# Performance work log

Hardware: AMD Instinct MI355X
Metric: run time of the kernel (lower is better)

Reference implementation:

```python
import jax, jax.numpy as jnp
import numpy as np

N_NODES = 100000
N_EDGES = 1600000
N_GRAPHS = 256
NEG_SLOPE_GAT = 0.2   # GATConv default
NEG_SLOPE_ACT = 0.01  # F.leaky_relu default


def _leaky(x, s):
    return jnp.where(x >= 0, x, s * x)


def _gat_layer(x, src, dst, W, a_src, a_dst, b, n):
    # h = W x ; per-node attention logits
    h = x @ W                      # [N, D]
    al_s = h @ a_src               # [N]
    al_d = h @ a_dst               # [N]
    e = _leaky(al_s[src] + al_d[dst], NEG_SLOPE_GAT)  # [E]
    # segment softmax over incoming edges of each dst node
    m = jax.ops.segment_max(e, dst, num_segments=n)
    m = jnp.where(jnp.isfinite(m), m, 0.0)
    ex = jnp.exp(e - m[dst])
    s = jax.ops.segment_sum(ex, dst, num_segments=n)
    alpha = ex / (s[dst] + 1e-16)
    out = jax.ops.segment_sum(h[src] * alpha[:, None], dst, num_segments=n)
    return out + b


def setup_inputs() -> dict:
    key = jax.random.key(0)
    ks = jax.random.split(key, 12)
    x = jax.random.normal(ks[0], (N_NODES, 72), dtype=jnp.float32)
    edge_index = jax.random.randint(ks[1], (2, N_EDGES), 0, N_NODES, dtype=jnp.int64)
    batch = jnp.sort(jax.random.randint(ks[2], (N_NODES,), 0, N_GRAPHS, dtype=jnp.int64))
    def glorot(k, shape):
        fan = shape[0] + shape[-1]
        return jax.random.normal(k, shape, dtype=jnp.float32) * jnp.sqrt(2.0 / fan)
    return {
        "x": x, "edge_index": edge_index, "batch": batch,
        "W1": glorot(ks[3], (72, 64)),
        "a_src1": glorot(ks[4], (64,)), "a_dst1": glorot(ks[5], (64,)),
        "b1": jnp.zeros((64,), jnp.float32),
        "W2": glorot(ks[6], (64, 64)),
        "a_src2": glorot(ks[7], (64,)), "a_dst2": glorot(ks[8], (64,)),
        "b2": jnp.zeros((64,), jnp.float32),
        "fcW": glorot(ks[9], (64, 2)),
        "fcb": jnp.zeros((2,), jnp.float32),
    }


def reference(x, edge_index, batch, W1, a_src1, a_dst1, b1, W2, a_src2, a_dst2, b2, fcW, fcb):
    n = x.shape[0]
    # PyG GATConv adds self-loops by default
    loops = jnp.arange(n, dtype=edge_index.dtype)
    src = jnp.concatenate([edge_index[0], loops])
    dst = jnp.concatenate([edge_index[1], loops])
    h = _gat_layer(x, src, dst, W1, a_src1, a_dst1, b1, n)
    h = _leaky(h, NEG_SLOPE_ACT)
    h = _gat_layer(h, src, dst, W2, a_src2, a_dst2, b2, n)
    # global mean pool over graphs
    sums = jax.ops.segment_sum(h, batch, num_segments=N_GRAPHS)
    cnt = jax.ops.segment_sum(jnp.ones((n,), h.dtype), batch, num_segments=N_GRAPHS)
    pooled = sums / jnp.maximum(cnt, 1.0)[:, None]
    # dropout is identity at inference
    return pooled @ fcW + fcb
```

## Files before the change

kernel.cpp:

```cpp
#include <hip/hip_runtime.h>
#include <hip/hip_bf16.h>
#include <math.h>


#define NPB 256
#define EPB 4096

__device__ __forceinline__ void atomAddF(float* a, float v) {
    unsafeAtomicAdd(a, v);
}

__device__ __forceinline__ unsigned int f2bf(float v) {
    unsigned int b = __float_as_uint(v);
    b += 0x7FFFu + ((b >> 16) & 1u);
    return b >> 16;
}

__global__ __launch_bounds__(256) void init_all(float* __restrict__ pooled,
                                                float* __restrict__ cnt,
                                                int* __restrict__ bucket_cnt,
                                                int NB, int G) {
    int i = blockIdx.x * 256 + threadIdx.x;
    if (i < G * 64) pooled[i] = 0.0f;
    if (i < G) cnt[i] = 0.0f;
    if (i < NB) bucket_cnt[i] = 0;
}

__global__ __launch_bounds__(256) void bucket_hist(const int* __restrict__ ei,
                                                   int E, int NB,
                                                   int* __restrict__ bucket_cnt) {
    __shared__ int h[512];
    int t = threadIdx.x;
    for (int i = t; i < 512; i += 256) h[i] = 0;
    __syncthreads();
    int i0 = blockIdx.x * EPB;
#pragma unroll
    for (int k = 0; k < 16; k++) {
        int i = i0 + k * 256 + t;
        if (i < E) atomicAdd(&h[ei[E + i] >> 8], 1);
    }
    __syncthreads();
    for (int b = t; b < NB; b += 256)
        if (h[b]) atomicAdd(&bucket_cnt[b], h[b]);
}

__global__ __launch_bounds__(512) void scan_buckets(const int* __restrict__ cnt,
                                                    int* __restrict__ base,
                                                    int* __restrict__ cur, int NB) {
    __shared__ int tmp[512];
    int t = threadIdx.x;
    int v = (t < NB) ? cnt[t] : 0;
    tmp[t] = v;
    __syncthreads();
    for (int o = 1; o < 512; o <<= 1) {
        int u = (t >= o) ? tmp[t - o] : 0;
        __syncthreads();
        tmp[t] += u;
        __syncthreads();
    }
    if (t < NB) { int e = tmp[t] - v; base[t] = e; cur[t] = e; }
}

__global__ __launch_bounds__(256) void partition(const int* __restrict__ ei,
                                                 int E, int NB,
                                                 int* __restrict__ cur,
                                                 uint2* __restrict__ pairs) {
    __shared__ int h[512];
    __shared__ int bb[512];
    int t = threadIdx.x;
    for (int i = t; i < 512; i += 256) h[i] = 0;
    __syncthreads();
    int i0 = blockIdx.x * EPB;
    int s[16], bk[16], r[16];
#pragma unroll
    for (int k = 0; k < 16; k++) {
        int i = i0 + k * 256 + t;
        bk[k] = -1;
        if (i < E) {
            s[k] = ei[i];
            int d = ei[E + i];
            bk[k] = d >> 8;
            r[k] = atomicAdd(&h[bk[k]], 1);
        }
    }
    __syncthreads();
    for (int b = t; b < NB; b += 256)
        bb[b] = h[b] ? atomicAdd(&cur[b], h[b]) : 0;
    __syncthreads();
#pragma unroll
    for (int k = 0; k < 16; k++) {
        if (bk[k] < 0) continue;
        int i = i0 + k * 256 + t;
        int d = ei[E + i];
        pairs[bb[bk[k]] + r[k]] = make_uint2((unsigned)s[k], (unsigned)d);
    }
}

__global__ __launch_bounds__(256) void build_csr(const uint2* __restrict__ pairs,
                                                 const int* __restrict__ cnt,
                                                 const int* __restrict__ base,
                                                 int n, int tot,
                                                 int* __restrict__ rowptr,
                                                 int* __restrict__ srcs) {
    int b = blockIdx.x, t = threadIdx.x;
    int d0 = b << 8;
    int nb = min(NPB, n - d0);
    int pbeg = base[b], pend = pbeg + cnt[b];
    int csr0 = pbeg + d0;

    __shared__ int deg[NPB];
    __shared__ int cur[NPB];
    __shared__ int tmp[NPB];
    deg[t] = (t < nb) ? 1 : 0;
    __syncthreads();
    for (int j = pbeg + t; j < pend; j += 256)
        atomicAdd(&deg[pairs[j].y - d0], 1);
    __syncthreads();
    int v = deg[t];
    tmp[t] = v;
    __syncthreads();
    for (int o = 1; o < NPB; o <<= 1) {
        int u = (t >= o) ? tmp[t - o] : 0;
        __syncthreads();
        tmp[t] += u;
        __syncthreads();
    }
    int excl = tmp[t] - v;
    if (t < nb) {
        rowptr[d0 + t] = csr0 + excl;
        srcs[csr0 + excl] = d0 + t;
        cur[t] = excl + 1;
    }
    __syncthreads();
    for (int j = pbeg + t; j < pend; j += 256) {
        uint2 p = pairs[j];
        int off = atomicAdd(&cur[p.y - d0], 1);
        srcs[csr0 + off] = (int)p.x;
    }
    if (b == 0 && t == 0) rowptr[n] = tot;
}

template <int IN_DIM>
__global__ __launch_bounds__(256) void node_gemm(const float* __restrict__ x,
                                                 const float* __restrict__ W,
                                                 const float* __restrict__ a_src,
                                                 const float* __restrict__ a_dst,
                                                 const float* __restrict__ bias_in,
                                                 float slope_in,
                                                 unsigned short* __restrict__ h16,
                                                 float* __restrict__ al_s,
                                                 float* __restrict__ al_d,
                                                 int n) {
    __shared__ float Ws[IN_DIM * 64];
    __shared__ float xs[IN_DIM][64];
    int t = threadIdx.x;
    int nbase = blockIdx.x * 64;

    for (int idx = t; idx < IN_DIM * 16; idx += 256)
        ((float4*)Ws)[idx] = ((const float4*)W)[idx];
    for (int idx = t; idx < IN_DIM * 64; idx += 256) {
        int node = nbase + (idx & 63);
        int k = idx >> 6;
        float v = 0.0f;
        if (node < n) {
            v = x[(size_t)node * IN_DIM + k];
            if (bias_in) {
                v += bias_in[k];
                v = (v >= 0.0f) ? v : slope_in * v;
            }
        }
        xs[k][idx & 63] = v;
    }
    __syncthreads();

    int cg = t & 15;
    int ng = t >> 4;
    float acc[4][4] = {};
#pragma unroll 8
    for (int k = 0; k < IN_DIM; k++) {
        float4 xv = *(const float4*)&xs[k][ng * 4];
        float4 wv = *(const float4*)&Ws[k * 64 + cg * 4];
        float xa[4] = {xv.x, xv.y, xv.z, xv.w};
        float wa[4] = {wv.x, wv.y, wv.z, wv.w};
#pragma unroll
        for (int i = 0; i < 4; i++)
#pragma unroll
            for (int j = 0; j < 4; j++)
                acc[i][j] += xa[i] * wa[j];
    }

    float4 as4 = *(const float4*)(a_src + cg * 4);
    float4 ad4 = *(const float4*)(a_dst + cg * 4);
#pragma unroll
    for (int i = 0; i < 4; i++) {
        int node = nbase + ng * 4 + i;
        if (node < n) {
            uint2 p;
            p.x = f2bf(acc[i][0]) | (f2bf(acc[i][1]) << 16);
            p.y = f2bf(acc[i][2]) | (f2bf(acc[i][3]) << 16);
            *(uint2*)(h16 + (size_t)node * 64 + cg * 4) = p;
        }
        float vs = acc[i][0] * as4.x + acc[i][1] * as4.y +
                   acc[i][2] * as4.z + acc[i][3] * as4.w;
        float vd = acc[i][0] * ad4.x + acc[i][1] * ad4.y +
                   acc[i][2] * ad4.z + acc[i][3] * ad4.w;
#pragma unroll
        for (int o = 8; o; o >>= 1) {
            vs += __shfl_xor(vs, o);
            vd += __shfl_xor(vd, o);
        }
        if (cg == 0 && node < n) { al_s[node] = vs; al_d[node] = vd; }
    }
}

__device__ __forceinline__ void bf8_fma(float* acc, uint4 q, float w) {
    acc[0] += w * __uint_as_float(q.x << 16);
    acc[1] += w * __uint_as_float(q.x & 0xFFFF0000u);
    acc[2] += w * __uint_as_float(q.y << 16);
    acc[3] += w * __uint_as_float(q.y & 0xFFFF0000u);
    acc[4] += w * __uint_as_float(q.z << 16);
    acc[5] += w * __uint_as_float(q.z & 0xFFFF0000u);
    acc[6] += w * __uint_as_float(q.w << 16);
    acc[7] += w * __uint_as_float(q.w & 0xFFFF0000u);
}

__global__ __launch_bounds__(256) void gat_aggregate(const int* __restrict__ rowptr,
                                                     const int* __restrict__ srcs,
                                                     const float* __restrict__ als,
                                                     const float* __restrict__ ald,
                                                     const unsigned short* __restrict__ h16,
                                                     float* __restrict__ hout,
                                                     int n) {
    int t = threadIdx.x;
    int sub = t >> 3, lane = t & 7;
    int node = blockIdx.x * 32 + sub;
    if (node >= n) return;
    int beg = rowptr[node], end = rowptr[node + 1];
    float aldv = ald[node];

    float acc[8] = {};
    float sm = 0.0f;
    int j = beg;
    for (; j + 4 <= end; j += 4) {
        int s0 = srcs[j], s1 = srcs[j + 1], s2 = srcs[j + 2], s3 = srcs[j + 3];
        float e0 = als[s0] + aldv, e1 = als[s1] + aldv;
        float e2 = als[s2] + aldv, e3 = als[s3] + aldv;
        uint4 q0 = *(const uint4*)(h16 + (size_t)s0 * 64 + lane * 8);
        uint4 q1 = *(const uint4*)(h16 + (size_t)s1 * 64 + lane * 8);
        uint4 q2 = *(const uint4*)(h16 + (size_t)s2 * 64 + lane * 8);
        uint4 q3 = *(const uint4*)(h16 + (size_t)s3 * 64 + lane * 8);
        e0 = (e0 >= 0.0f) ? e0 : 0.2f * e0;
        e1 = (e1 >= 0.0f) ? e1 : 0.2f * e1;
        e2 = (e2 >= 0.0f) ? e2 : 0.2f * e2;
        e3 = (e3 >= 0.0f) ? e3 : 0.2f * e3;
        float w0 = __expf(e0), w1 = __expf(e1);
        float w2 = __expf(e2), w3 = __expf(e3);
        sm += (w0 + w1) + (w2 + w3);
        bf8_fma(acc, q0, w0);
        bf8_fma(acc, q1, w1);
        bf8_fma(acc, q2, w2);
        bf8_fma(acc, q3, w3);
    }
    for (; j < end; j++) {
        int s = srcs[j];
        float e = als[s] + aldv;
        e = (e >= 0.0f) ? e : 0.2f * e;
        float w = __expf(e);
        uint4 q = *(const uint4*)(h16 + (size_t)s * 64 + lane * 8);
        sm += w;
        bf8_fma(acc, q, w);
    }

    float inv = 1.0f / (sm + 1e-16f);
    float4 o0 = make_float4(acc[0] * inv, acc[1] * inv, acc[2] * inv, acc[3] * inv);
    float4 o1 = make_float4(acc[4] * inv, acc[5] * inv, acc[6] * inv, acc[7] * inv);
    float* op = hout + (size_t)node * 64 + lane * 8;
    *(float4*)op = o0;
    *(float4*)(op + 4) = o1;
}

__global__ __launch_bounds__(256) void pool_run(const float* __restrict__ hout,
                                                const float* __restrict__ b2,
                                                const int* __restrict__ batch,
                                                float* __restrict__ pooled,
                                                float* __restrict__ cnt,
                                                int n) {
    int t = threadIdx.x;
    int wv = blockIdx.x * 4 + (t >> 6);
    int lane = t & 63;
    int start = wv * 64;
    if (start >= n) return;
    int end = min(start + 64, n);
    float bb = b2[lane];
    int gcur = batch[start];
    float acc = 0.0f;
    int rl = 0;
    for (int node = start; node < end; node++) {
        int g = batch[node];
        if (g != gcur) {
            atomAddF(&pooled[gcur * 64 + lane], acc);
            if (lane == 0) atomAddF(&cnt[gcur], (float)rl);
            acc = 0.0f; rl = 0; gcur = g;
        }
        acc += hout[(size_t)node * 64 + lane] + bb;
        rl++;
    }
    atomAddF(&pooled[gcur * 64 + lane], acc);
    if (lane == 0) atomAddF(&cnt[gcur], (float)rl);
}

__global__ __launch_bounds__(64) void final_fc(const float* __restrict__ pooled,
                                               const float* __restrict__ cnt,
                                               const float* __restrict__ fcW,
                                               const float* __restrict__ fcb,
                                               float* __restrict__ out) {
    int g = blockIdx.x;
    int lane = threadIdx.x;
    float c = cnt[g];
    c = (c > 1.0f) ? c : 1.0f;
    float p = pooled[g * 64 + lane] / c;
    float s0 = p * fcW[lane * 2 + 0];
    float s1 = p * fcW[lane * 2 + 1];
#pragma unroll
    for (int o = 32; o; o >>= 1) {
        s0 += __shfl_xor(s0, o);
        s1 += __shfl_xor(s1, o);
    }
    if (lane == 0) {
        out[g * 2 + 0] = s0 + fcb[0];
        out[g * 2 + 1] = s1 + fcb[1];
    }
}

extern "C" void kernel_launch(void* const* d_in, const int* in_sizes, int n_in,
                              void* d_out, int out_size, void* d_ws, size_t ws_size,
                              hipStream_t stream) {
    const float* x    = (const float*)d_in[0];
    const int*   ei   = (const int*)d_in[1];
    const int*   batch= (const int*)d_in[2];
    const float* W1   = (const float*)d_in[3];
    const float* as1  = (const float*)d_in[4];
    const float* ad1  = (const float*)d_in[5];
    const float* b1   = (const float*)d_in[6];
    const float* W2   = (const float*)d_in[7];
    const float* as2  = (const float*)d_in[8];
    const float* ad2  = (const float*)d_in[9];
    const float* b2   = (const float*)d_in[10];
    const float* fcW  = (const float*)d_in[11];
    const float* fcb  = (const float*)d_in[12];
    float* out = (float*)d_out;

    const int N = in_sizes[2];
    const int E = in_sizes[1] / 2;
    const int G = out_size / 2;
    const int tot = E + N;
    const int NB = (N + NPB - 1) / NPB;

    float* ws     = (float*)d_ws;
    float* bufO   = ws;
    uint2* pairs  = (uint2*)(bufO + (size_t)N * 64);
    float* als    = (float*)(pairs + E);
    float* ald    = als + N;
    float* pooled = ald + N;
    float* cnt    = pooled + (size_t)G * 64;
    int*   rowptr = (int*)(cnt + G);
    int*   srcs   = rowptr + N + 1;
    int*   bcnt   = srcs + tot;
    int*   bbase  = bcnt + NB;
    int*   bcur   = bbase + NB;
    unsigned short* bufH16 = (unsigned short*)(bcur + NB);

    dim3 b256(256);
    int gInit = (max(G * 64, NB) + 255) / 256;
    int gPart = (E + EPB - 1) / EPB;
    int gGemm = (N + 63) / 64;
    int gAgg  = (N + 31) / 32;
    int gPool = ((N + 63) / 64 + 3) / 4;

    init_all<<<gInit, b256, 0, stream>>>(pooled, cnt, bcnt, NB, G);
    bucket_hist<<<gPart, b256, 0, stream>>>(ei, E, NB, bcnt);
    scan_buckets<<<1, 512, 0, stream>>>(bcnt, bbase, bcur, NB);
    partition<<<gPart, b256, 0, stream>>>(ei, E, NB, bcur, pairs);
    build_csr<<<NB, b256, 0, stream>>>(pairs, bcnt, bbase, N, tot, rowptr, srcs);

    node_gemm<72><<<gGemm, b256, 0, stream>>>(x, W1, as1, ad1, nullptr, 0.0f,
                                              bufH16, als, ald, N);
    gat_aggregate<<<gAgg, b256, 0, stream>>>(rowptr, srcs, als, ald, bufH16, bufO, N);

    node_gemm<64><<<gGemm, b256, 0, stream>>>(bufO, W2, as2, ad2, b1, 0.01f,
                                              bufH16, als, ald, N);
    gat_aggregate<<<gAgg, b256, 0, stream>>>(rowptr, srcs, als, ald, bufH16, bufO, N);

    pool_run<<<gPool, b256, 0, stream>>>(bufO, b2, batch, pooled, cnt, N);
    final_fc<<<G, 64, 0, stream>>>(pooled, cnt, fcW, fcb, out);
}
```

Measured before the change: 348.9 us.

## Precompute edge weights and sort nodes by degree for balanced aggregation

Adds a separate edge_weights pass that computes exp(leaky(als[src]+ald[dst])) per edge and stores it packed with the source index. The aggregation kernel then reads these packed pairs instead of recomputing logits. It also builds a degree-bucketed permutation of nodes (histogram, scan, scatter), so each block's 8-lane groups handle nodes of similar degree, reducing load imbalance within wavefronts. The cost is extra kernel launches and an additional pass over the edges that writes and rereads 8 bytes per edge. The permutation also scatters output writes.

```diff
diff --git a/kernel.cpp b/kernel.cpp
--- a/kernel.cpp
+++ b/kernel.cpp
@@ -19,11 +19,13 @@
 __global__ __launch_bounds__(256) void init_all(float* __restrict__ pooled,
                                                 float* __restrict__ cnt,
                                                 int* __restrict__ bucket_cnt,
+                                                int* __restrict__ bins,
                                                 int NB, int G) {
     int i = blockIdx.x * 256 + threadIdx.x;
     if (i < G * 64) pooled[i] = 0.0f;
     if (i < G) cnt[i] = 0.0f;
     if (i < NB) bucket_cnt[i] = 0;
+    if (i < 64) bins[i] = 0;
 }
 
 __global__ __launch_bounds__(256) void bucket_hist(const int* __restrict__ ei,
@@ -138,6 +140,57 @@
         srcs[csr0 + off] = (int)p.x;
     }
     if (b == 0 && t == 0) rowptr[n] = tot;
+}
+
+__global__ __launch_bounds__(256) void perm_hist(const int* __restrict__ rowptr,
+                                                 int n, int* __restrict__ bins) {
+    __shared__ int h[64];
+    int t = threadIdx.x;
+    if (t < 64) h[t] = 0;
+    __syncthreads();
+    int i = blockIdx.x * 256 + t;
+    if (i < n) {
+        int d = min(rowptr[i + 1] - rowptr[i], 64) - 1;
+        atomicAdd(&h[d], 1);
+    }
+    __syncthreads();
+    if (t < 64 && h[t]) atomicAdd(&bins[t], h[t]);
+}
+
+__global__ __launch_bounds__(64) void perm_scan(const int* __restrict__ bins,
+                                                int* __restrict__ cur) {
+    __shared__ int tmp[64];
+    int t = threadIdx.x;
+    int v = bins[t];
+    tmp[t] = v;
+    __syncthreads();
+    for (int o = 1; o < 64; o <<= 1) {
+        int u = (t >= o) ? tmp[t - o] : 0;
+        __syncthreads();
+        tmp[t] += u;
+        __syncthreads();
+    }
+    cur[t] = tmp[t] - v;
+}
+
+__global__ __launch_bounds__(256) void perm_scatter(const int* __restrict__ rowptr,
+                                                    int n, int* __restrict__ cur,
+                                                    int* __restrict__ perm) {
+    __shared__ int h[64];
+    __shared__ int bb[64];
+    int t = threadIdx.x;
+    if (t < 64) h[t] = 0;
+    __syncthreads();
+    int i = blockIdx.x * 256 + t;
+    int b = -1, r = 0;
+    if (i < n) {
+        b = min(rowptr[i + 1] - rowptr[i], 64) - 1;
+        r = atomicAdd(&h[b], 1);
+    }
+    __syncthreads();
+    if (t < 64) bb[t] = h[t] ? atomicAdd(&cur[t], h[t]) : 0;
+    __syncthreads();
+    if (i < n) perm[bb[b] + r] = i;
 }
 
 template <int IN_DIM>
@@ -213,6 +266,25 @@
     }
 }
 
+__global__ __launch_bounds__(256) void edge_weights(const int* __restrict__ rowptr,
+                                                    const int* __restrict__ srcs,
+                                                    const float* __restrict__ als,
+                                                    const float* __restrict__ ald,
+                                                    uint2* __restrict__ ew, int n) {
+    int t = threadIdx.x;
+    int sub = t >> 3, lane = t & 7;
+    int node = blockIdx.x * 32 + sub;
+    if (node >= n) return;
+    float adv = ald[node];
+    int beg = rowptr[node], end = rowptr[node + 1];
+    for (int j = beg + lane; j < end; j += 8) {
+        int s = srcs[j];
+        float e = als[s] + adv;
+        e = (e >= 0.0f) ? e : 0.2f * e;
+        ew[j] = make_uint2((unsigned)s, __float_as_uint(__expf(e)));
+    }
+}
+
 __device__ __forceinline__ void bf8_fma(float* acc, uint4 q, float w) {
     acc[0] += w * __uint_as_float(q.x << 16);
     acc[1] += w * __uint_as_float(q.x & 0xFFFF0000u);
@@ -225,36 +297,29 @@
 }
 
 __global__ __launch_bounds__(256) void gat_aggregate(const int* __restrict__ rowptr,
-                                                     const int* __restrict__ srcs,
-                                                     const float* __restrict__ als,
-                                                     const float* __restrict__ ald,
+                                                     const int* __restrict__ perm,
+                                                     const uint2* __restrict__ ew,
                                                      const unsigned short* __restrict__ h16,
                                                      float* __restrict__ hout,
                                                      int n) {
     int t = threadIdx.x;
     int sub = t >> 3, lane = t & 7;
-    int node = blockIdx.x * 32 + sub;
-    if (node >= n) return;
+    int r = blockIdx.x * 32 + sub;
+    if (r >= n) return;
+    int node = perm[r];
     int beg = rowptr[node], end = rowptr[node + 1];
-    float aldv = ald[node];
 
     float acc[8] = {};
     float sm = 0.0f;
     int j = beg;
     for (; j + 4 <= end; j += 4) {
-        int s0 = srcs[j], s1 = srcs[j + 1], s2 = srcs[j + 2], s3 = srcs[j + 3];
-        float e0 = als[s0] + aldv, e1 = als[s1] + aldv;
-        float e2 = als[s2] + aldv, e3 = als[s3] + aldv;
-        uint4 q0 = *(const uint4*)(h16 + (size_t)s0 * 64 + lane * 8);
-        uint4 q1 = *(const uint4*)(h16 + (size_t)s1 * 64 + lane * 8);
-        uint4 q2 = *(const uint4*)(h16 + (size_t)s2 * 64 + lane * 8);
-        uint4 q3 = *(const uint4*)(h16 + (size_t)s3 * 64 + lane * 8);
-        e0 = (e0 >= 0.0f) ? e0 : 0.2f * e0;
-        e1 = (e1 >= 0.0f) ? e1 : 0.2f * e1;
-        e2 = (e2 >= 0.0f) ? e2 : 0.2f * e2;
-        e3 = (e3 >= 0.0f) ? e3 : 0.2f * e3;
-        float w0 = __expf(e0), w1 = __expf(e1);
-        float w2 = __expf(e2), w3 = __expf(e3);
+        uint2 e0 = ew[j], e1 = ew[j + 1], e2 = ew[j + 2], e3 = ew[j + 3];
+        uint4 q0 = *(const uint4*)(h16 + (size_t)e0.x * 64 + lane * 8);
+        uint4 q1 = *(const uint4*)(h16 + (size_t)e1.x * 64 + lane * 8);
+        uint4 q2 = *(const uint4*)(h16 + (size_t)e2.x * 64 + lane * 8);
+        uint4 q3 = *(const uint4*)(h16 + (size_t)e3.x * 64 + lane * 8);
+        float w0 = __uint_as_float(e0.y), w1 = __uint_as_float(e1.y);
+        float w2 = __uint_as_float(e2.y), w3 = __uint_as_float(e3.y);
         sm += (w0 + w1) + (w2 + w3);
         bf8_fma(acc, q0, w0);
         bf8_fma(acc, q1, w1);
@@ -262,11 +327,9 @@
         bf8_fma(acc, q3, w3);
     }
     for (; j < end; j++) {
-        int s = srcs[j];
-        float e = als[s] + aldv;
-        e = (e >= 0.0f) ? e : 0.2f * e;
-        float w = __expf(e);
-        uint4 q = *(const uint4*)(h16 + (size_t)s * 64 + lane * 8);
+        uint2 e = ew[j];
+        float w = __uint_as_float(e.y);
+        uint4 q = *(const uint4*)(h16 + (size_t)e.x * 64 + lane * 8);
         sm += w;
         bf8_fma(acc, q, w);
     }
@@ -359,7 +422,8 @@
     float* ws     = (float*)d_ws;
     float* bufO   = ws;
     uint2* pairs  = (uint2*)(bufO + (size_t)N * 64);
-    float* als    = (float*)(pairs + E);
+    uint2* ew     = pairs;
+    float* als    = (float*)(pairs + tot);
     float* ald    = als + N;
     float* pooled = ald + N;
     float* cnt    = pooled + (size_t)G * 64;
@@ -368,28 +432,37 @@
     int*   bcnt   = srcs + tot;
     int*   bbase  = bcnt + NB;
     int*   bcur   = bbase + NB;
-    unsigned short* bufH16 = (unsigned short*)(bcur + NB);
+    int*   bins   = bcur + NB;
+    int*   pcur   = bins + 64;
+    int*   perm   = pcur + 64;
+    unsigned short* bufH16 = (unsigned short*)(perm + N);
 
     dim3 b256(256);
     int gInit = (max(G * 64, NB) + 255) / 256;
     int gPart = (E + EPB - 1) / EPB;
+    int gNB   = (N + 255) / 256;
     int gGemm = (N + 63) / 64;
     int gAgg  = (N + 31) / 32;
     int gPool = ((N + 63) / 64 + 3) / 4;
 
-    init_all<<<gInit, b256, 0, stream>>>(pooled, cnt, bcnt, NB, G);
+    init_all<<<gInit, b256, 0, stream>>>(pooled, cnt, bcnt, bins, NB, G);
     bucket_hist<<<gPart, b256, 0, stream>>>(ei, E, NB, bcnt);
     scan_buckets<<<1, 512, 0, stream>>>(bcnt, bbase, bcur, NB);
     partition<<<gPart, b256, 0, stream>>>(ei, E, NB, bcur, pairs);
     build_csr<<<NB, b256, 0, stream>>>(pairs, bcnt, bbase, N, tot, rowptr, srcs);
+    perm_hist<<<gNB, b256, 0, stream>>>(rowptr, N, bins);
+    perm_scan<<<1, 64, 0, stream>>>(bins, pcur);
+    perm_scatter<<<gNB, b256, 0, stream>>>(rowptr, N, pcur, perm);
 
     node_gemm<72><<<gGemm, b256, 0, stream>>>(x, W1, as1, ad1, nullptr, 0.0f,
                                               bufH16, als, ald, N);
-    gat_aggregate<<<gAgg, b256, 0, stream>>>(rowptr, srcs, als, ald, bufH16, bufO, N);
+    edge_weights<<<gAgg, b256, 0, stream>>>(rowptr, srcs, als, ald, ew, N);
+    gat_aggregate<<<gAgg, b256, 0, stream>>>(rowptr, perm, ew, bufH16, bufO, N);
 
     node_gemm<64><<<gGemm, b256, 0, stream>>>(bufO, W2, as2, ad2, b1, 0.01f,
                                               bufH16, als, ald, N);
-    gat_aggregate<<<gAgg, b256, 0, stream>>>(rowptr, srcs, als, ald, bufH16, bufO, N);
+    edge_weights<<<gAgg, b256, 0, stream>>>(rowptr, srcs, als, ald, ew, N);
+    gat_aggregate<<<gAgg, b256, 0, stream>>>(rowptr, perm, ew, bufH16, bufO, N);
 
     pool_run<<<gPool, b256, 0, stream>>>(bufO, b2, batch, pooled, cnt, N);
     final_fc<<<G, 64, 0, stream>>>(pooled, cnt, fcW, fcb, out);
```

After: 400.7 us. 14.9% more time.

## Split GAT aggregation into two feature-half passes with 4 lanes per node

Applied to the files above, without the earlier changes.

The aggregation kernel now handles half of the 64 features per launch, with 4 threads per node instead of 8, and runs twice per layer (phase 0 and 1). The aim is to shrink the gathered working set per pass (32 bf16 features per source row) so it fits better in cache during the random gathers. The cost is that the edge list, attention logits and exp are read and computed twice, and there are extra kernel launches.

```diff
diff --git a/kernel.cpp b/kernel.cpp
--- a/kernel.cpp
+++ b/kernel.cpp
@@ -224,19 +224,21 @@
     acc[7] += w * __uint_as_float(q.w & 0xFFFF0000u);
 }
 
-__global__ __launch_bounds__(256) void gat_aggregate(const int* __restrict__ rowptr,
-                                                     const int* __restrict__ srcs,
-                                                     const float* __restrict__ als,
-                                                     const float* __restrict__ ald,
-                                                     const unsigned short* __restrict__ h16,
-                                                     float* __restrict__ hout,
-                                                     int n) {
-    int t = threadIdx.x;
-    int sub = t >> 3, lane = t & 7;
-    int node = blockIdx.x * 32 + sub;
+__global__ __launch_bounds__(256) void gat_aggregate_half(
+        const int* __restrict__ rowptr,
+        const int* __restrict__ srcs,
+        const float* __restrict__ als,
+        const float* __restrict__ ald,
+        const unsigned short* __restrict__ h16,
+        float* __restrict__ hout,
+        int n, int phase) {
+    int t = threadIdx.x;
+    int sub = t >> 2, lane = t & 3;
+    int node = blockIdx.x * 64 + sub;
     if (node >= n) return;
     int beg = rowptr[node], end = rowptr[node + 1];
     float aldv = ald[node];
+    const unsigned short* hb = h16 + phase * 32 + lane * 8;
 
     float acc[8] = {};
     float sm = 0.0f;
@@ -245,10 +247,10 @@
         int s0 = srcs[j], s1 = srcs[j + 1], s2 = srcs[j + 2], s3 = srcs[j + 3];
         float e0 = als[s0] + aldv, e1 = als[s1] + aldv;
         float e2 = als[s2] + aldv, e3 = als[s3] + aldv;
-        uint4 q0 = *(const uint4*)(h16 + (size_t)s0 * 64 + lane * 8);
-        uint4 q1 = *(const uint4*)(h16 + (size_t)s1 * 64 + lane * 8);
-        uint4 q2 = *(const uint4*)(h16 + (size_t)s2 * 64 + lane * 8);
-        uint4 q3 = *(const uint4*)(h16 + (size_t)s3 * 64 + lane * 8);
+        uint4 q0 = *(const uint4*)(hb + (size_t)s0 * 64);
+        uint4 q1 = *(const uint4*)(hb + (size_t)s1 * 64);
+        uint4 q2 = *(const uint4*)(hb + (size_t)s2 * 64);
+        uint4 q3 = *(const uint4*)(hb + (size_t)s3 * 64);
         e0 = (e0 >= 0.0f) ? e0 : 0.2f * e0;
         e1 = (e1 >= 0.0f) ? e1 : 0.2f * e1;
         e2 = (e2 >= 0.0f) ? e2 : 0.2f * e2;
@@ -266,7 +268,7 @@
         float e = als[s] + aldv;
         e = (e >= 0.0f) ? e : 0.2f * e;
         float w = __expf(e);
-        uint4 q = *(const uint4*)(h16 + (size_t)s * 64 + lane * 8);
+        uint4 q = *(const uint4*)(hb + (size_t)s * 64);
         sm += w;
         bf8_fma(acc, q, w);
     }
@@ -274,7 +276,7 @@
     float inv = 1.0f / (sm + 1e-16f);
     float4 o0 = make_float4(acc[0] * inv, acc[1] * inv, acc[2] * inv, acc[3] * inv);
     float4 o1 = make_float4(acc[4] * inv, acc[5] * inv, acc[6] * inv, acc[7] * inv);
-    float* op = hout + (size_t)node * 64 + lane * 8;
+    float* op = hout + (size_t)node * 64 + phase * 32 + lane * 8;
     *(float4*)op = o0;
     *(float4*)(op + 4) = o1;
 }
@@ -374,7 +376,7 @@
     int gInit = (max(G * 64, NB) + 255) / 256;
     int gPart = (E + EPB - 1) / EPB;
     int gGemm = (N + 63) / 64;
-    int gAgg  = (N + 31) / 32;
+    int gAggH = (N + 63) / 64;
     int gPool = ((N + 63) / 64 + 3) / 4;
 
     init_all<<<gInit, b256, 0, stream>>>(pooled, cnt, bcnt, NB, G);
@@ -385,11 +387,17 @@
 
     node_gemm<72><<<gGemm, b256, 0, stream>>>(x, W1, as1, ad1, nullptr, 0.0f,
                                               bufH16, als, ald, N);
-    gat_aggregate<<<gAgg, b256, 0, stream>>>(rowptr, srcs, als, ald, bufH16, bufO, N);
+    gat_aggregate_half<<<gAggH, b256, 0, stream>>>(rowptr, srcs, als, ald,
+                                                   bufH16, bufO, N, 0);
+    gat_aggregate_half<<<gAggH, b256, 0, stream>>>(rowptr, srcs, als, ald,
+                                                   bufH16, bufO, N, 1);
 
     node_gemm<64><<<gGemm, b256, 0, stream>>>(bufO, W2, as2, ad2, b1, 0.01f,
                                               bufH16, als, ald, N);
-    gat_aggregate<<<gAgg, b256, 0, stream>>>(rowptr, srcs, als, ald, bufH16, bufO, N);
+    gat_aggregate_half<<<gAggH, b256, 0, stream>>>(rowptr, srcs, als, ald,
+                                                   bufH16, bufO, N, 0);
+    gat_aggregate_half<<<gAggH, b256, 0, stream>>>(rowptr, srcs, als, ald,
+                                                   bufH16, bufO, N, 1);
 
     pool_run<<<gPool, b256, 0, stream>>>(bufO, b2, batch, pooled, cnt, N);
     final_fc<<<G, 64, 0, stream>>>(pooled, cnt, fcW, fcb, out);
```

After: 421.9 us. +20.9%, slower.
